# Performance work log

Measured on AMD Instinct MI355X. Metric: run time of the kernel, lower is better.

The kernel has to match this reference:

```python
import jax, jax.numpy as jnp
import numpy as np

D_IN = 1024
D_EMB = 512
HIDDEN = 256
NUM_CLASSES = 64
N_SUPPORT = 4096
N_QUERY = 8192


def setup_inputs() -> dict:
    key = jax.random.key(0)
    ks = jax.random.split(key, 8)
    scale_e = 1.0 / np.sqrt(D_IN)
    scale_1 = 1.0 / np.sqrt(2 * D_EMB)
    scale_2 = 1.0 / np.sqrt(HIDDEN)
    return {
        "support_data": jax.random.normal(ks[0], (N_SUPPORT, D_IN), jnp.float32),
        "query_data": jax.random.normal(ks[1], (N_QUERY, D_IN), jnp.float32),
        "support_label": jax.random.randint(ks[2], (N_SUPPORT,), 0, NUM_CLASSES, jnp.int32),
        "W_e": jax.random.normal(ks[3], (D_IN, D_EMB), jnp.float32) * scale_e,
        "b_e": jnp.zeros((D_EMB,), jnp.float32),
        "W1": jax.random.normal(ks[4], (2 * D_EMB, HIDDEN), jnp.float32) * scale_1,
        "b1": jnp.zeros((HIDDEN,), jnp.float32),
        "W2": jax.random.normal(ks[5], (HIDDEN, 1), jnp.float32) * scale_2,
        "b2": jnp.zeros((1,), jnp.float32),
    }


def reference(support_data, query_data, support_label, W_e, b_e, W1, b1, W2, b2):
    # embedding_net: Linear + ReLU
    s_emb = jax.nn.relu(support_data @ W_e + b_e)  # [Ns, D_EMB]
    q_emb = jax.nn.relu(query_data @ W_e + b_e)    # [Nq, D_EMB]

    # per-class mean of support embeddings (segment mean; labels are 0..C-1,
    # matching torch.unique()'s sorted order)
    sums = jax.ops.segment_sum(s_emb, support_label, num_segments=NUM_CLASSES)
    counts = jax.ops.segment_sum(jnp.ones((s_emb.shape[0],), s_emb.dtype),
                                 support_label, num_segments=NUM_CLASSES)
    means = sums / jnp.maximum(counts, 1.0)[:, None]  # [C, D_EMB]

    # relation_net on concat(query, class_mean): split first linear so the
    # [Nq*C, 2*D_EMB] concat is never materialized (same math).
    Wq, Wc = W1[:D_EMB], W1[D_EMB:]
    h = jax.nn.relu(q_emb @ Wq[:, None, :].squeeze(1) @ jnp.eye(HIDDEN, dtype=W1.dtype)
                    if False else
                    (q_emb @ Wq)[:, None, :] + (means @ Wc)[None, :, :] + b1)  # [Nq, C, HIDDEN]
    scores = jax.nn.sigmoid(h @ W2 + b2)  # [Nq, C, 1]
    # torch version stacks [1,1]-shaped scores -> [Nq, C, 1, 1]
    return scores[:, :, None, :]
```

## Files before the change

kernel.cpp:

```cpp
#include <hip/hip_runtime.h>
#include <hip/hip_bf16.h>

#define D_IN 1024
#define D_EMB 512
#define HIDDEN 256
#define NUM_CLASSES 64
#define N_SUPPORT 4096
#define N_QUERY 8192

typedef __bf16 bf16x8 __attribute__((ext_vector_type(8)));
typedef __bf16 bf16x4 __attribute__((ext_vector_type(4)));
typedef float f32x4 __attribute__((ext_vector_type(4)));

#define GLOAD_LDS16(g, l)                                                          \
  __builtin_amdgcn_global_load_lds(                                                \
      (const __attribute__((address_space(1))) unsigned int*)(g),                  \
      (__attribute__((address_space(3))) unsigned int*)(l), 16, 0, 0)

__global__ __launch_bounds__(256) void prep(
    const float* __restrict__ W_e, const float* __restrict__ W1,
    const float* __restrict__ support, const float* __restrict__ query,
    __bf16* __restrict__ WeT, __bf16* __restrict__ WqT,
    __bf16* __restrict__ Xbf) {
  const int tid = threadIdx.x;
  int b = blockIdx.x;
  if (b < 640) {
    __shared__ float tile[32][33];
    const float* in;
    __bf16* out;
    int bx, by, rows, cols;
    if (b < 512) {
      in = W_e; out = WeT; rows = D_IN; cols = D_EMB;
      bx = (b & 15) * 32; by = (b >> 4) * 32;
    } else {
      b -= 512;
      in = W1; out = WqT; rows = D_EMB; cols = HIDDEN;
      bx = (b & 7) * 32; by = (b >> 3) * 32;
    }
    int tx = tid & 31, ty = tid >> 5;
#pragma unroll
    for (int i = ty; i < 32; i += 8)
      tile[i][tx] = in[(long)(by + i) * cols + bx + tx];
    __syncthreads();
#pragma unroll
    for (int i = ty; i < 32; i += 8)
      out[(long)(bx + i) * rows + by + tx] = (__bf16)tile[tx][i];
  } else {
    const long nsup = (long)N_SUPPORT * D_IN;
    long base = (long)(b - 640) * 4096;
#pragma unroll
    for (int g = 0; g < 4; ++g) {
      long i = base + g * 1024 + tid * 4;
      const float* src = (i < nsup) ? (support + i) : (query + (i - nsup));
      float4 v = *(const float4*)src;
      bf16x4 o;
      o[0] = (__bf16)v.x; o[1] = (__bf16)v.y;
      o[2] = (__bf16)v.z; o[3] = (__bf16)v.w;
      *(bf16x4*)(Xbf + i) = o;
    }
  }
}

__global__ __launch_bounds__(256, 3) void gemm_emb(
    const __bf16* __restrict__ A, const __bf16* __restrict__ BT,
    const float* __restrict__ bias, __bf16* __restrict__ C) {
  constexpr int BM = 128, BN = 64, BK = 64;
  constexpr int N = D_EMB, K = D_IN;
  constexpr int NT = K / BK;
  constexpr int MR = 4, NR = 2;

  __shared__ __align__(16) __bf16 As[2][BM * BK];
  __shared__ __align__(16) __bf16 Bs[2][BN * BK];

  const int tid = threadIdx.x;
  const int wave = tid >> 6, lane = tid & 63;
  const int wr = wave >> 1, wc = wave & 1;
  const int l16 = lane & 15, half = lane >> 4;
  const int r7 = l16 & 7;

  const int m0 = blockIdx.x * BM;
  const int n0 = blockIdx.y * BN;

  const __bf16* aptr[4];
#pragma unroll
  for (int q = 0; q < 4; ++q) {
    int chunk = q * 256 + tid;
    int row = chunk >> 3;
    int kc = (chunk & 7) ^ (row & 7);
    aptr[q] = A + (long)(m0 + row) * K + kc * 8;
  }
  const __bf16* bptr[2];
#pragma unroll
  for (int q = 0; q < 2; ++q) {
    int chunk = q * 256 + tid;
    int row = chunk >> 3;
    int kc = (chunk & 7) ^ (row & 7);
    bptr[q] = BT + (long)(n0 + row) * K + kc * 8;
  }

  f32x4 acc[MR][NR];
#pragma unroll
  for (int m = 0; m < MR; ++m)
#pragma unroll
    for (int n = 0; n < NR; ++n) acc[m][n] = (f32x4)0.0f;

#define STAGE(t, buf)                                                       \
  {                                                                         \
    _Pragma("unroll") for (int q = 0; q < 4; ++q)                           \
        GLOAD_LDS16(aptr[q] + (t) * BK, &As[buf][(q * 256 + tid) * 8]);     \
    _Pragma("unroll") for (int q = 0; q < 2; ++q)                           \
        GLOAD_LDS16(bptr[q] + (t) * BK, &Bs[buf][(q * 256 + tid) * 8]);     \
  }

#define COMPUTE(buf)                                                        \
  {                                                                         \
    bf16x8 a[MR][2], b[NR][2];                                              \
    _Pragma("unroll") for (int m = 0; m < MR; ++m) {                        \
      int row = wr * 64 + m * 16 + l16;                                     \
      _Pragma("unroll") for (int ks = 0; ks < 2; ++ks)                      \
          a[m][ks] = *(const bf16x8*)(&As[buf][row * BK +                   \
                                      (((ks * 4 + half) ^ r7) * 8)]);       \
    }                                                                       \
    _Pragma("unroll") for (int n = 0; n < NR; ++n) {                        \
      int row = wc * 32 + n * 16 + l16;                                     \
      _Pragma("unroll") for (int ks = 0; ks < 2; ++ks)                      \
          b[n][ks] = *(const bf16x8*)(&Bs[buf][row * BK +                   \
                                      (((ks * 4 + half) ^ r7) * 8)]);       \
    }                                                                       \
    asm volatile("s_waitcnt lgkmcnt(0)" ::: "memory");                      \
    __builtin_amdgcn_sched_barrier(0);                                      \
    _Pragma("unroll") for (int ks = 0; ks < 2; ++ks)                        \
        _Pragma("unroll") for (int m = 0; m < MR; ++m)                      \
            _Pragma("unroll") for (int n = 0; n < NR; ++n)                  \
                acc[m][n] = __builtin_amdgcn_mfma_f32_16x16x32_bf16(        \
                    a[m][ks], b[n][ks], acc[m][n], 0, 0, 0);                \
  }

  STAGE(0, 0);
  asm volatile("s_waitcnt vmcnt(0)" ::: "memory");
  __builtin_amdgcn_s_barrier();

  int cur = 0;
  for (int t = 0; t < NT - 1; ++t) {
    STAGE(t + 1, cur ^ 1);
    COMPUTE(cur);
    asm volatile("s_waitcnt vmcnt(0)" ::: "memory");
    __builtin_amdgcn_s_barrier();
    cur ^= 1;
  }
  COMPUTE(cur);

#undef STAGE
#undef COMPUTE

#pragma unroll
  for (int m = 0; m < MR; ++m)
#pragma unroll
    for (int n = 0; n < NR; ++n) {
      const int col = n0 + wc * 32 + n * 16 + l16;
      const float bv = bias[col];
#pragma unroll
      for (int j = 0; j < 4; ++j) {
        int row = m0 + wr * 64 + m * 16 + half * 4 + j;
        float v = fmaxf(acc[m][n][j] + bv, 0.0f);
        C[(long)row * N + col] = (__bf16)v;
      }
    }
}

__global__ __launch_bounds__(256, 4) void qp_proto(
    const __bf16* __restrict__ emb, const __bf16* __restrict__ BT,
    const float* __restrict__ bias, float* __restrict__ Cqp,
    const int* __restrict__ labels, float* __restrict__ sums_part,
    int* __restrict__ cnt_part) {
  constexpr int BM = 64, BN = 64, BK = 32;
  constexpr int N = HIDDEN, K = D_EMB;
  constexpr int NT = K / BK;
  constexpr int MR = 2, NR = 2;

  __shared__ __align__(16) __bf16 As[4][BM * BK];
  __shared__ __align__(16) __bf16 Bs[4][BN * BK];

  const int tid = threadIdx.x;
  const int bid = blockIdx.x;

  if (bid >= 512) {
    const int pb = bid - 512;
    const int c = pb >> 3;
    const int s = pb & 7;
    const int j0 = s * (N_SUPPORT / 8);
    float a0 = 0.0f, a1 = 0.0f;
    int count = 0;
#pragma unroll 4
    for (int j = j0; j < j0 + N_SUPPORT / 8; j += 4) {
      int4 lab4 = *(const int4*)(labels + j);
#pragma unroll
      for (int u = 0; u < 4; ++u) {
        int lab = (u == 0) ? lab4.x : (u == 1) ? lab4.y : (u == 2) ? lab4.z : lab4.w;
        if (lab == c) {
          const __bf16* r = emb + (long)(j + u) * D_EMB;
          a0 += (float)r[tid];
          a1 += (float)r[tid + 256];
          ++count;
        }
      }
    }
    float* dst = sums_part + (long)(c * 8 + s) * D_EMB;
    dst[tid] = a0;
    dst[tid + 256] = a1;
    if (tid == 0) cnt_part[c * 8 + s] = count;
    return;
  }

  const __bf16* A = emb + (long)N_SUPPORT * D_EMB;
  const int wave = tid >> 6, lane = tid & 63;
  const int wr = wave >> 1, wc = wave & 1;
  const int l16 = lane & 15, half = lane >> 4;
  const int slot = half ^ ((l16 >> 1) & 3);

  const int m0 = (bid & 127) * BM;
  const int n0 = (bid >> 7) * BN;

  const int srow = tid >> 2;
  const int skc = (tid & 3) ^ ((srow >> 1) & 3);
  const __bf16* aptr = A + (long)(m0 + srow) * K + skc * 8;
  const __bf16* bptr = BT + (long)(n0 + srow) * K + skc * 8;

  f32x4 acc[MR][NR];
#pragma unroll
  for (int m = 0; m < MR; ++m)
#pragma unroll
    for (int n = 0; n < NR; ++n) acc[m][n] = (f32x4)0.0f;

#define STAGE(t, buf)                                                       \
  {                                                                         \
    GLOAD_LDS16(aptr + (t) * BK, &As[buf][tid * 8]);                        \
    GLOAD_LDS16(bptr + (t) * BK, &Bs[buf][tid * 8]);                        \
  }

#define COMPUTE(buf)                                                        \
  {                                                                         \
    bf16x8 a[MR], b[NR];                                                    \
    _Pragma("unroll") for (int m = 0; m < MR; ++m)                          \
        a[m] = *(const bf16x8*)(&As[buf][(wr * 32 + m * 16 + l16) * BK +    \
                                         slot * 8]);                        \
    _Pragma("unroll") for (int n = 0; n < NR; ++n)                          \
        b[n] = *(const bf16x8*)(&Bs[buf][(wc * 32 + n * 16 + l16) * BK +    \
                                         slot * 8]);                        \
    asm volatile("s_waitcnt lgkmcnt(0)" ::: "memory");                      \
    __builtin_amdgcn_sched_barrier(0);                                      \
    _Pragma("unroll") for (int m = 0; m < MR; ++m)                          \
        _Pragma("unroll") for (int n = 0; n < NR; ++n)                      \
            acc[m][n] = __builtin_amdgcn_mfma_f32_16x16x32_bf16(            \
                a[m], b[n], acc[m][n], 0, 0, 0);                            \
  }

  STAGE(0, 0);
  STAGE(1, 1);
  STAGE(2, 2);
  asm volatile("s_waitcnt vmcnt(4)" ::: "memory");
  __builtin_amdgcn_s_barrier();

  for (int t = 0; t < NT - 3; ++t) {
    STAGE(t + 3, (t + 3) & 3);
    COMPUTE(t & 3);
    asm volatile("s_waitcnt vmcnt(4)" ::: "memory");
    __builtin_amdgcn_s_barrier();
  }
  COMPUTE((NT - 3) & 3);
  asm volatile("s_waitcnt vmcnt(2)" ::: "memory");
  __builtin_amdgcn_s_barrier();
  COMPUTE((NT - 2) & 3);
  asm volatile("s_waitcnt vmcnt(0)" ::: "memory");
  __builtin_amdgcn_s_barrier();
  COMPUTE((NT - 1) & 3);

#undef STAGE
#undef COMPUTE

#pragma unroll
  for (int m = 0; m < MR; ++m)
#pragma unroll
    for (int n = 0; n < NR; ++n) {
      const int col = n0 + wc * 32 + n * 16 + l16;
      const float bv = bias[col];
#pragma unroll
      for (int j = 0; j < 4; ++j) {
        int row = m0 + wr * 32 + m * 16 + half * 4 + j;
        Cqp[(long)row * N + col] = acc[m][n][j] + bv;
      }
    }
}

__global__ __launch_bounds__(256) void proto_cpb(
    const float* __restrict__ sums_part, const int* __restrict__ cnt_part,
    const float* __restrict__ W1, float* __restrict__ cpb_part) {
  __shared__ float ls[128];
  const int c = blockIdx.x;
  const int kc = blockIdx.y;
  const int k0 = kc * 128;
  const int tid = threadIdx.x;

  int nc = 0;
#pragma unroll
  for (int s = 0; s < 8; ++s) nc += cnt_part[c * 8 + s];
  float inv = 1.0f / fmaxf((float)nc, 1.0f);

  if (tid < 128) {
    float v = 0.0f;
#pragma unroll
    for (int s = 0; s < 8; ++s)
      v += sums_part[(long)(c * 8 + s) * D_EMB + k0 + tid];
    ls[tid] = v * inv;
  }
  __syncthreads();

  float acc = 0.0f;
#pragma unroll 8
  for (int k = 0; k < 128; ++k)
    acc = fmaf(ls[k], W1[(long)(D_EMB + k0 + k) * HIDDEN + tid], acc);
  cpb_part[((long)kc * NUM_CLASSES + c) * HIDDEN + tid] = acc;
}

__global__ __launch_bounds__(256) void score_kernel(
    const float* __restrict__ qp, const float* __restrict__ cpb_part,
    const float* __restrict__ W2, const float* __restrict__ b2,
    float* __restrict__ out) {
  constexpr int CPB_S = 260;
  __shared__ __align__(16) float cpb_s[NUM_CLASSES * CPB_S];
  __shared__ __align__(16) float qp_s[32 * HIDDEN];
  __shared__ __align__(16) float w2_s[HIDDEN];

  const int tid = threadIdx.x;
  const int w = tid >> 6;
  const int c = tid & 63;
  const int qb0 = blockIdx.x * 32;
  constexpr int NCH = NUM_CLASSES * HIDDEN;

  w2_s[tid] = W2[tid];
  for (int i = tid; i < NCH; i += 256)
    cpb_s[(i >> 8) * CPB_S + (i & (HIDDEN - 1))] =
        cpb_part[i] + cpb_part[NCH + i] + cpb_part[2 * NCH + i] +
        cpb_part[3 * NCH + i];
  for (int i = tid; i < 32 * HIDDEN; i += 256)
    qp_s[i] = qp[(long)qb0 * HIDDEN + i];
  __syncthreads();

  const float bb = b2[0];
  float acc[8];
#pragma unroll
  for (int q = 0; q < 8; ++q) acc[q] = 0.0f;

  const float* crow = cpb_s + c * CPB_S;
  const float* qbase = qp_s + (w * 8) * HIDDEN;

#pragma unroll 4
  for (int kc = 0; kc < HIDDEN / 4; ++kc) {
    f32x4 cv = *(const f32x4*)(crow + kc * 4);
    f32x4 wv = *(const f32x4*)(w2_s + kc * 4);
#pragma unroll
    for (int q = 0; q < 8; ++q) {
      f32x4 qv = *(const f32x4*)(qbase + q * HIDDEN + kc * 4);
      acc[q] = fmaf(fmaxf(qv[0] + cv[0], 0.0f), wv[0], acc[q]);
      acc[q] = fmaf(fmaxf(qv[1] + cv[1], 0.0f), wv[1], acc[q]);
      acc[q] = fmaf(fmaxf(qv[2] + cv[2], 0.0f), wv[2], acc[q]);
      acc[q] = fmaf(fmaxf(qv[3] + cv[3], 0.0f), wv[3], acc[q]);
    }
  }

#pragma unroll
  for (int q = 0; q < 8; ++q) {
    float x = acc[q] + bb;
    out[(long)(qb0 + w * 8 + q) * NUM_CLASSES + c] = 1.0f / (1.0f + __expf(-x));
  }
}

extern "C" void kernel_launch(void* const* d_in, const int* in_sizes, int n_in,
                              void* d_out, int out_size, void* d_ws,
                              size_t ws_size, hipStream_t stream) {
  const float* support = (const float*)d_in[0];
  const float* query   = (const float*)d_in[1];
  const int*   labels  = (const int*)d_in[2];
  const float* W_e     = (const float*)d_in[3];
  const float* b_e     = (const float*)d_in[4];
  const float* W1      = (const float*)d_in[5];
  const float* b1      = (const float*)d_in[6];
  const float* W2      = (const float*)d_in[7];
  const float* b2      = (const float*)d_in[8];
  float* out = (float*)d_out;

  char* ws = (char*)d_ws;
  size_t off = 0;
  auto alloc = [&](size_t bytes) {
    void* p = ws + off;
    off = (off + bytes + 255) & ~(size_t)255;
    return p;
  };
  const long NTOT = N_SUPPORT + N_QUERY;
  __bf16* Xbf = (__bf16*)alloc((size_t)NTOT * D_IN * 2);
  __bf16* WeT = (__bf16*)alloc((size_t)D_EMB * D_IN * 2);
  __bf16* WqT = (__bf16*)alloc((size_t)HIDDEN * D_EMB * 2);
  __bf16* emb = (__bf16*)alloc((size_t)NTOT * D_EMB * 2);
  float*  qp  = (float*)alloc((size_t)N_QUERY * HIDDEN * 4);
  float*  sums_part = (float*)alloc((size_t)NUM_CLASSES * 8 * D_EMB * 4);
  int*    cnt_part  = (int*)alloc((size_t)NUM_CLASSES * 8 * 4);
  float*  cpb_part  = (float*)alloc((size_t)4 * NUM_CLASSES * HIDDEN * 4);

  prep<<<640 + (int)(NTOT * D_IN / 4096), 256, 0, stream>>>(
      W_e, W1, support, query, WeT, WqT, Xbf);

  gemm_emb<<<dim3(NTOT / 128, D_EMB / 64), 256, 0, stream>>>(
      Xbf, WeT, b_e, emb);

  qp_proto<<<1024, 256, 0, stream>>>(emb, WqT, b1, qp, labels, sums_part,
                                     cnt_part);

  proto_cpb<<<dim3(NUM_CLASSES, 4), 256, 0, stream>>>(sums_part, cnt_part, W1,
                                                      cpb_part);

  score_kernel<<<N_QUERY / 32, 256, 0, stream>>>(qp, cpb_part, W2, b2, out);
}
```

Before: 82.05 us.

## Double K tile to 64 and switch qp_proto to two-stage double buffering

Raises the K tile of the query projection GEMM from 32 to 64 and replaces the four-deep LDS ring with a two-buffer ping-pong, with a new XOR swizzle suited to 64-wide rows. Each iteration now issues two MFMAs per A/B fragment pair across the two k-substeps, halving the number of barriers and loop iterations. The trade-off is a shallower prefetch (one stage ahead, with a full vmcnt(0) wait each step), which may expose more global-load latency.

Result: slower. 83.78 us (+2.1%).

```diff
diff --git a/kernel.cpp b/kernel.cpp
--- a/kernel.cpp
+++ b/kernel.cpp
@@ -173,13 +173,13 @@
     const float* __restrict__ bias, float* __restrict__ Cqp,
     const int* __restrict__ labels, float* __restrict__ sums_part,
     int* __restrict__ cnt_part) {
-  constexpr int BM = 64, BN = 64, BK = 32;
+  constexpr int BM = 64, BN = 64, BK = 64;
   constexpr int N = HIDDEN, K = D_EMB;
   constexpr int NT = K / BK;
   constexpr int MR = 2, NR = 2;
 
-  __shared__ __align__(16) __bf16 As[4][BM * BK];
-  __shared__ __align__(16) __bf16 Bs[4][BN * BK];
+  __shared__ __align__(16) __bf16 As[2][BM * BK];
+  __shared__ __align__(16) __bf16 Bs[2][BN * BK];
 
   const int tid = threadIdx.x;
   const int bid = blockIdx.x;
@@ -216,15 +216,21 @@
   const int wave = tid >> 6, lane = tid & 63;
   const int wr = wave >> 1, wc = wave & 1;
   const int l16 = lane & 15, half = lane >> 4;
-  const int slot = half ^ ((l16 >> 1) & 3);
+  const int r7 = l16 & 7;
 
   const int m0 = (bid & 127) * BM;
   const int n0 = (bid >> 7) * BN;
 
-  const int srow = tid >> 2;
-  const int skc = (tid & 3) ^ ((srow >> 1) & 3);
-  const __bf16* aptr = A + (long)(m0 + srow) * K + skc * 8;
-  const __bf16* bptr = BT + (long)(n0 + srow) * K + skc * 8;
+  const __bf16* aptr[2];
+  const __bf16* bptr[2];
+#pragma unroll
+  for (int q = 0; q < 2; ++q) {
+    int chunk = q * 256 + tid;
+    int row = chunk >> 3;
+    int kc = (chunk & 7) ^ (row & 7);
+    aptr[q] = A + (long)(m0 + row) * K + kc * 8;
+    bptr[q] = BT + (long)(n0 + row) * K + kc * 8;
+  }
 
   f32x4 acc[MR][NR];
 #pragma unroll
@@ -234,46 +240,49 @@
 
 #define STAGE(t, buf)                                                       \
   {                                                                         \
-    GLOAD_LDS16(aptr + (t) * BK, &As[buf][tid * 8]);                        \
-    GLOAD_LDS16(bptr + (t) * BK, &Bs[buf][tid * 8]);                        \
+    _Pragma("unroll") for (int q = 0; q < 2; ++q) {                         \
+      GLOAD_LDS16(aptr[q] + (t) * BK, &As[buf][(q * 256 + tid) * 8]);       \
+      GLOAD_LDS16(bptr[q] + (t) * BK, &Bs[buf][(q * 256 + tid) * 8]);       \
+    }                                                                       \
   }
 
 #define COMPUTE(buf)                                                        \
   {                                                                         \
-    bf16x8 a[MR], b[NR];                                                    \
-    _Pragma("unroll") for (int m = 0; m < MR; ++m)                          \
-        a[m] = *(const bf16x8*)(&As[buf][(wr * 32 + m * 16 + l16) * BK +    \
-                                         slot * 8]);                        \
-    _Pragma("unroll") for (int n = 0; n < NR; ++n)                          \
-        b[n] = *(const bf16x8*)(&Bs[buf][(wc * 32 + n * 16 + l16) * BK +    \
-                                         slot * 8]);                        \
+    bf16x8 a[MR][2], b[NR][2];                                              \
+    _Pragma("unroll") for (int m = 0; m < MR; ++m) {                        \
+      int row = wr * 32 + m * 16 + l16;                                     \
+      _Pragma("unroll") for (int ks = 0; ks < 2; ++ks)                      \
+          a[m][ks] = *(const bf16x8*)(&As[buf][row * BK +                   \
+                                      (((ks * 4 + half) ^ r7) * 8)]);       \
+    }                                                                       \
+    _Pragma("unroll") for (int n = 0; n < NR; ++n) {                        \
+      int row = wc * 32 + n * 16 + l16;                                     \
+      _Pragma("unroll") for (int ks = 0; ks < 2; ++ks)                      \
+          b[n][ks] = *(const bf16x8*)(&Bs[buf][row * BK +                   \
+                                      (((ks * 4 + half) ^ r7) * 8)]);       \
+    }                                                                       \
     asm volatile("s_waitcnt lgkmcnt(0)" ::: "memory");                      \
     __builtin_amdgcn_sched_barrier(0);                                      \
-    _Pragma("unroll") for (int m = 0; m < MR; ++m)                          \
-        _Pragma("unroll") for (int n = 0; n < NR; ++n)                      \
-            acc[m][n] = __builtin_amdgcn_mfma_f32_16x16x32_bf16(            \
-                a[m], b[n], acc[m][n], 0, 0, 0);                            \
+    _Pragma("unroll") for (int ks = 0; ks < 2; ++ks)                        \
+        _Pragma("unroll") for (int m = 0; m < MR; ++m)                      \
+            _Pragma("unroll") for (int n = 0; n < NR; ++n)                  \
+                acc[m][n] = __builtin_amdgcn_mfma_f32_16x16x32_bf16(        \
+                    a[m][ks], b[n][ks], acc[m][n], 0, 0, 0);                \
   }
 
   STAGE(0, 0);
-  STAGE(1, 1);
-  STAGE(2, 2);
-  asm volatile("s_waitcnt vmcnt(4)" ::: "memory");
-  __builtin_amdgcn_s_barrier();
-
-  for (int t = 0; t < NT - 3; ++t) {
-    STAGE(t + 3, (t + 3) & 3);
-    COMPUTE(t & 3);
-    asm volatile("s_waitcnt vmcnt(4)" ::: "memory");
-    __builtin_amdgcn_s_barrier();
-  }
-  COMPUTE((NT - 3) & 3);
-  asm volatile("s_waitcnt vmcnt(2)" ::: "memory");
-  __builtin_amdgcn_s_barrier();
-  COMPUTE((NT - 2) & 3);
   asm volatile("s_waitcnt vmcnt(0)" ::: "memory");
   __builtin_amdgcn_s_barrier();
-  COMPUTE((NT - 1) & 3);
+
+  int cur = 0;
+  for (int t = 0; t < NT - 1; ++t) {
+    STAGE(t + 1, cur ^ 1);
+    COMPUTE(cur);
+    asm volatile("s_waitcnt vmcnt(0)" ::: "memory");
+    __builtin_amdgcn_s_barrier();
+    cur ^= 1;
+  }
+  COMPUTE(cur);
 
 #undef STAGE
 #undef COMPUTE
```
